# Kernel tuning notes

Measured on AMD Instinct MI355X. Metric: run time of the kernel, lower is better.

The kernel has to match this reference:

```python
import jax, jax.numpy as jnp
import numpy as np

N_NODES = 50000
N_EDGES = 800000
HID = 256
HEADS = 4
HEAD_C = HID // HEADS  # 64
IN_CH = 16
OUT_CH = 4
NEG_SLOPE = 0.2  # PyG GATConv default LeakyReLU slope
LN_EPS = 1e-5


def setup_inputs() -> dict:
    key = jax.random.key(0)
    ks = jax.random.split(key, 12)
    s = 0.05
    return {
        "x": jax.random.normal(ks[0], (N_NODES, IN_CH), dtype=jnp.float32),
        "edge_index": jax.random.randint(ks[1], (2, N_EDGES), 0, N_NODES, dtype=jnp.int64),
        "w_in": jax.random.normal(ks[2], (IN_CH, HID), dtype=jnp.float32) * s,
        "b_in": jnp.zeros((HID,), dtype=jnp.float32),
        "w_gat": jax.random.normal(ks[3], (4, HID, HID), dtype=jnp.float32) * s,
        "att_src": jax.random.normal(ks[4], (4, HEADS, HEAD_C), dtype=jnp.float32) * s,
        "att_dst": jax.random.normal(ks[5], (4, HEADS, HEAD_C), dtype=jnp.float32) * s,
        "b_gat": jnp.zeros((4, HID), dtype=jnp.float32),
        "ln_scale": jnp.ones((4, HID), dtype=jnp.float32),
        "ln_bias": jnp.zeros((4, HID), dtype=jnp.float32),
        "w_out": jax.random.normal(ks[6], (HID, OUT_CH), dtype=jnp.float32) * s,
        "b_out": jnp.zeros((OUT_CH,), dtype=jnp.float32),
    }


def _gat_layer(x, src, dst, W, a_src, a_dst, bias, g, beta):
    """One GATConv(concat, heads=4) + LayerNorm + ELU. x:[N,HID]."""
    n = x.shape[0]
    h = (x @ W).reshape(n, HEADS, HEAD_C)                 # [N,H,C]
    a_s = jnp.einsum("nhc,hc->nh", h, a_src)              # [N,H]
    a_d = jnp.einsum("nhc,hc->nh", h, a_dst)              # [N,H]
    logits = jax.nn.leaky_relu(a_s[src] + a_d[dst], NEG_SLOPE)  # [E,H]
    # segment softmax over destination neighborhoods (self-loops ensure non-empty)
    m = jax.ops.segment_max(logits, dst, num_segments=n)
    e = jnp.exp(logits - m[dst])
    denom = jax.ops.segment_sum(e, dst, num_segments=n)
    alpha = e / (denom[dst] + 1e-16)                      # [E,H]
    msg = alpha[:, :, None] * h[src]                      # [E,H,C]
    out = jax.ops.segment_sum(msg, dst, num_segments=n).reshape(n, HID) + bias
    mu = out.mean(-1, keepdims=True)
    var = out.var(-1, keepdims=True)
    out = (out - mu) * jax.lax.rsqrt(var + LN_EPS) * g + beta
    return jax.nn.elu(out)


def reference(x, edge_index, w_in, b_in, w_gat, att_src, att_dst, b_gat,
              ln_scale, ln_bias, w_out, b_out):
    n = x.shape[0]
    # PyG GATConv adds self-loops by default
    loops = jnp.arange(n, dtype=edge_index.dtype)
    ei = jnp.concatenate([edge_index, jnp.stack([loops, loops])], axis=1)
    src, dst = ei[0], ei[1]

    x = x @ w_in + b_in                                   # input_proj
    h = x
    for l in (0, 1):
        h = _gat_layer(h, src, dst, w_gat[l], att_src[l], att_dst[l],
                       b_gat[l], ln_scale[l], ln_bias[l])
    x = x + h
    h = x
    for l in (2, 3):
        h = _gat_layer(h, src, dst, w_gat[l], att_src[l], att_dst[l],
                       b_gat[l], ln_scale[l], ln_bias[l])
    x = x + h
    return x @ w_out + b_out
```

## Files before the change

kernel.cpp:

```cpp
#include <hip/hip_runtime.h>
#include <math.h>

#define NN 50000
#define E0 800000
#define ET 850000
#define HID 256
#define INCH 16
#define MAXDEG 64

#define NB_EDGE 3321
#define NB_WT   256
#define NB_IP   6250
#define NB_PREP (NB_EDGE + NB_WT + NB_IP)

typedef _Float16 h8 __attribute__((ext_vector_type(8)));
typedef float f32x4 __attribute__((ext_vector_type(4)));

__device__ __forceinline__ void load_lds16(const void* g, void* l) {
    __builtin_amdgcn_global_load_lds(
        (const __attribute__((address_space(1))) unsigned int*)g,
        (__attribute__((address_space(3))) unsigned int*)l, 16, 0, 0);
}

__global__ __launch_bounds__(256) void prep_kernel(
    const int* __restrict__ ei, int* __restrict__ cursor, int* __restrict__ csr_pad,
    const float* __restrict__ w_gat, _Float16* __restrict__ WT,
    const float* __restrict__ x, const float* __restrict__ w_in,
    const float* __restrict__ b_in, _Float16* __restrict__ Ph) {
    int b = blockIdx.x, t = threadIdx.x;
    if (b < NB_EDGE) {
        int e = b * 256 + t;
        if (e < ET) {
            int s, d;
            if (e < E0) { s = ei[e]; d = ei[E0 + e]; }
            else        { s = d = e - E0; }
            int pos = atomicAdd(&cursor[d], 1);
            if (pos < MAXDEG) csr_pad[(d << 6) + pos] = s;
        }
    } else if (b < NB_EDGE + NB_WT) {
        int k = b - NB_EDGE;
#pragma unroll
        for (int l = 0; l < 4; ++l) {
            float v = w_gat[((size_t)l * 256 + k) * 256 + t];
            WT[((size_t)l * 256 + t) * 256 + k] = (_Float16)v;
        }
    } else {
        int ipb = b - NB_EDGE - NB_WT;
        int sub = t >> 5, l32 = t & 31;
        int n = ipb * 8 + sub;
        int c0 = l32 * 8;
        const float* xr = x + n * INCH;
        float a[8];
#pragma unroll
        for (int k = 0; k < 8; k += 4) {
            float4 bb = *(const float4*)(b_in + c0 + k);
            a[k] = bb.x; a[k + 1] = bb.y; a[k + 2] = bb.z; a[k + 3] = bb.w;
        }
#pragma unroll
        for (int k = 0; k < INCH; ++k) {
            float xv = xr[k];
            const float4 w0 = *(const float4*)(w_in + k * 256 + c0);
            const float4 w1 = *(const float4*)(w_in + k * 256 + c0 + 4);
            a[0] += xv * w0.x; a[1] += xv * w0.y; a[2] += xv * w0.z; a[3] += xv * w0.w;
            a[4] += xv * w1.x; a[5] += xv * w1.y; a[6] += xv * w1.z; a[7] += xv * w1.w;
        }
        h8 o;
#pragma unroll
        for (int k = 0; k < 8; ++k) o[k] = (_Float16)a[k];
        *(h8*)(Ph + (size_t)n * 256 + c0) = o;
    }
}

__global__ __launch_bounds__(256) void gemm_fused_kernel(
    const _Float16* __restrict__ A, const _Float16* __restrict__ BT,
    _Float16* __restrict__ H, const float* __restrict__ att_s,
    const float* __restrict__ att_d, float* __restrict__ AS, float* __restrict__ AD,
    int N) {
    __shared__ _Float16 As[128 * 32];
    __shared__ _Float16 Bs[128 * 32];
    int t = threadIdx.x;
    int wv = t >> 6, lane = t & 63;
    int rb = blockIdx.x * 128, cb = blockIdx.y * 128;
    int wr = (wv >> 1) * 64, wc = (wv & 1) * 64;
    int lm = lane & 15, lq = lane >> 4;
    f32x4 acc[4][4] = {};

    int rch = lane >> 2;
    int q = lane & 3;

    for (int k0 = 0; k0 < 256; k0 += 32) {
#pragma unroll
        for (int c = 0; c < 2; ++c) {
            int r = wv * 32 + c * 16 + rch;
            int g = q ^ (r & 3);
            int ra = rb + r; if (ra >= N) ra = N - 1;
            load_lds16(A + (size_t)ra * 256 + k0 + g * 8,
                       (char*)As + wv * 2048 + c * 1024);
            load_lds16(BT + (size_t)(cb + r) * 256 + k0 + g * 8,
                       (char*)Bs + wv * 2048 + c * 1024);
        }
        __syncthreads();
        h8 af[4], bfr[4];
#pragma unroll
        for (int i = 0; i < 4; ++i) {
            int row = wr + i * 16 + lm;
            af[i] = *(const h8*)((const char*)As + row * 64 + ((lq ^ (row & 3)) * 16));
        }
#pragma unroll
        for (int j = 0; j < 4; ++j) {
            int row = wc + j * 16 + lm;
            bfr[j] = *(const h8*)((const char*)Bs + row * 64 + ((lq ^ (row & 3)) * 16));
        }
#pragma unroll
        for (int i = 0; i < 4; ++i)
#pragma unroll
            for (int j = 0; j < 4; ++j)
                acc[i][j] = __builtin_amdgcn_mfma_f32_16x16x32_f16(af[i], bfr[j], acc[i][j], 0, 0, 0);
        __syncthreads();
    }

    int head = (cb + wc) >> 6;
    float sa[4], sd[4];
#pragma unroll
    for (int j = 0; j < 4; ++j) {
        sa[j] = att_s[head * 64 + j * 16 + lm];
        sd[j] = att_d[head * 64 + j * 16 + lm];
    }
#pragma unroll
    for (int i = 0; i < 4; ++i)
#pragma unroll
        for (int rr = 0; rr < 4; ++rr) {
            float vs = acc[i][0][rr] * sa[0] + acc[i][1][rr] * sa[1]
                     + acc[i][2][rr] * sa[2] + acc[i][3][rr] * sa[3];
            float vd = acc[i][0][rr] * sd[0] + acc[i][1][rr] * sd[1]
                     + acc[i][2][rr] * sd[2] + acc[i][3][rr] * sd[3];
#pragma unroll
            for (int o = 1; o <= 8; o <<= 1) {
                vs += __shfl_xor(vs, o, 64);
                vd += __shfl_xor(vd, o, 64);
            }
            int row = rb + wr + i * 16 + lq * 4 + rr;
            if (lm == 0 && row < N) {
                AS[row * 4 + head] = vs;
                AD[row * 4 + head] = vd;
            }
        }

#pragma unroll
    for (int i = 0; i < 4; ++i)
#pragma unroll
        for (int j = 0; j < 4; ++j) {
            int col = cb + wc + j * 16 + lm;
#pragma unroll
            for (int rr = 0; rr < 4; ++rr) {
                int row = rb + wr + i * 16 + lq * 4 + rr;
                if (row < N) H[(size_t)row * 256 + col] = (_Float16)acc[i][j][rr];
            }
        }
}

__global__ __launch_bounds__(256) void agg_kernel(
    const _Float16* __restrict__ H, const float4* __restrict__ AS,
    const float4* __restrict__ AD,
    const int* __restrict__ cnt, const int* __restrict__ csr_pad,
    const float* __restrict__ bias, const float* __restrict__ g, const float* __restrict__ beta,
    const _Float16* __restrict__ res, _Float16* __restrict__ outh) {
    int t = threadIdx.x;
    int l32 = t & 31;
    int n = blockIdx.x * 8 + (t >> 5);
    int deg = cnt[n];
    if (deg > MAXDEG) deg = MAXDEG;
    int start = n << 6, end = start + deg;
    float4 adv = AD[n];
    int head = l32 >> 3;
    int c0 = l32 * 8;
    float advh = (head == 0) ? adv.x : (head == 1) ? adv.y : (head == 2) ? adv.z : adv.w;

    float acc[8] = {};
    float acc_e = 0.f;
#pragma unroll 4
    for (int i = start; i < end; ++i) {
        int s = csr_pad[i];
        const float* as = (const float*)&AS[s];
        float v = as[head] + advh;
        v = (v >= 0.f) ? v : 0.2f * v;
        float e = __expf(v);
        acc_e += e;
        h8 hv = *(const h8*)(H + (size_t)s * 256 + c0);
#pragma unroll
        for (int k = 0; k < 8; ++k) acc[k] += e * (float)hv[k];
    }
    float dinv = 1.f / (acc_e + 1e-16f);

    float val[8];
#pragma unroll
    for (int k = 0; k < 8; k += 4) {
        float4 bb = *(const float4*)(bias + c0 + k);
        val[k]     = acc[k]     * dinv + bb.x;
        val[k + 1] = acc[k + 1] * dinv + bb.y;
        val[k + 2] = acc[k + 2] * dinv + bb.z;
        val[k + 3] = acc[k + 3] * dinv + bb.w;
    }

    float s1 = 0.f, s2 = 0.f;
#pragma unroll
    for (int k = 0; k < 8; ++k) { s1 += val[k]; s2 += val[k] * val[k]; }
#pragma unroll
    for (int o = 16; o >= 1; o >>= 1) {
        s1 += __shfl_xor(s1, o, 64);
        s2 += __shfl_xor(s2, o, 64);
    }
    float mu = s1 * (1.f / 256.f);
    float var = s2 * (1.f / 256.f) - mu * mu;
    float rs = rsqrtf(var + 1e-5f);

    float y[8];
#pragma unroll
    for (int k = 0; k < 8; k += 4) {
        float4 g4 = *(const float4*)(g + c0 + k);
        float4 b4 = *(const float4*)(beta + c0 + k);
        y[k]     = (val[k]     - mu) * rs * g4.x + b4.x;
        y[k + 1] = (val[k + 1] - mu) * rs * g4.y + b4.y;
        y[k + 2] = (val[k + 2] - mu) * rs * g4.z + b4.z;
        y[k + 3] = (val[k + 3] - mu) * rs * g4.w + b4.w;
    }
#pragma unroll
    for (int k = 0; k < 8; ++k) y[k] = (y[k] > 0.f) ? y[k] : (__expf(y[k]) - 1.f);
    if (res) {
        h8 r0 = *(const h8*)(res + (size_t)n * 256 + c0);
#pragma unroll
        for (int k = 0; k < 8; ++k) y[k] += (float)r0[k];
    }
    h8 o0;
#pragma unroll
    for (int k = 0; k < 8; ++k) o0[k] = (_Float16)y[k];
    *(h8*)(outh + (size_t)n * 256 + c0) = o0;
}

__global__ __launch_bounds__(256) void out_proj_kernel(
    const _Float16* __restrict__ x, const float* __restrict__ w,
    const float* __restrict__ b, float* __restrict__ out, int n) {
    int tid = blockIdx.x * blockDim.x + threadIdx.x;
    int node = tid >> 6, lane = tid & 63;
    if (node >= n) return;
    const _Float16* xp = x + (size_t)node * HID + lane * 4;
    float x0 = (float)xp[0], x1 = (float)xp[1], x2 = (float)xp[2], x3 = (float)xp[3];
    const float4* wr = (const float4*)w;
    float4 w0 = wr[lane * 4 + 0];
    float4 w1 = wr[lane * 4 + 1];
    float4 w2 = wr[lane * 4 + 2];
    float4 w3 = wr[lane * 4 + 3];
    float o0 = x0 * w0.x + x1 * w1.x + x2 * w2.x + x3 * w3.x;
    float o1 = x0 * w0.y + x1 * w1.y + x2 * w2.y + x3 * w3.y;
    float o2 = x0 * w0.z + x1 * w1.z + x2 * w2.z + x3 * w3.z;
    float o3 = x0 * w0.w + x1 * w1.w + x2 * w2.w + x3 * w3.w;
#pragma unroll
    for (int o = 32; o >= 1; o >>= 1) {
        o0 += __shfl_down(o0, o, 64);
        o1 += __shfl_down(o1, o, 64);
        o2 += __shfl_down(o2, o, 64);
        o3 += __shfl_down(o3, o, 64);
    }
    if (lane == 0) {
        out[node * 4 + 0] = o0 + b[0];
        out[node * 4 + 1] = o1 + b[1];
        out[node * 4 + 2] = o2 + b[2];
        out[node * 4 + 3] = o3 + b[3];
    }
}

extern "C" void kernel_launch(void* const* d_in, const int* in_sizes, int n_in,
                              void* d_out, int out_size, void* d_ws, size_t ws_size,
                              hipStream_t stream) {
    const float* x       = (const float*)d_in[0];
    const int*   ei      = (const int*)  d_in[1];
    const float* w_in    = (const float*)d_in[2];
    const float* b_in    = (const float*)d_in[3];
    const float* w_gat   = (const float*)d_in[4];
    const float* att_src = (const float*)d_in[5];
    const float* att_dst = (const float*)d_in[6];
    const float* b_gat   = (const float*)d_in[7];
    const float* ln_g    = (const float*)d_in[8];
    const float* ln_b    = (const float*)d_in[9];
    const float* w_out   = (const float*)d_in[10];
    const float* b_out   = (const float*)d_in[11];
    float* out = (float*)d_out;

    char* ws = (char*)d_ws;
    size_t off = 0;
    auto alloc = [&](size_t bytes) {
        void* p = ws + off;
        off += (bytes + 255) & ~(size_t)255;
        return p;
    };
    _Float16*  Ph      = (_Float16*)alloc((size_t)NN * HID * 2);
    _Float16*  Ch      = (_Float16*)alloc((size_t)NN * HID * 2);
    _Float16*  Gh      = (_Float16*)alloc((size_t)NN * HID * 2);
    _Float16*  H       = (_Float16*)alloc((size_t)NN * HID * 2);
    _Float16*  WT      = (_Float16*)alloc((size_t)4 * HID * HID * 2);
    float*     ASAD    = (float*)alloc((size_t)NN * 8 * 4);
    int*       cursor  = (int*)alloc((size_t)NN * 4);
    int*       csr_pad = (int*)alloc((size_t)NN * MAXDEG * 4);

    float* AS = ASAD;
    float* AD = ASAD + (size_t)NN * 4;

    const dim3 GEMM_GRID((NN + 127) / 128, 2);
    const int NB_AGG = NN / 8;

    hipMemsetAsync(cursor, 0, (size_t)NN * 4, stream);
    prep_kernel<<<NB_PREP, 256, 0, stream>>>(ei, cursor, csr_pad, w_gat, WT,
                                             x, w_in, b_in, Ph);

    auto run_layer = [&](const _Float16* inh, int l, const _Float16* res, _Float16* outh) {
        gemm_fused_kernel<<<GEMM_GRID, 256, 0, stream>>>(
            inh, WT + (size_t)l * HID * HID, H,
            att_src + l * 256, att_dst + l * 256, AS, AD, NN);
        agg_kernel<<<NB_AGG, 256, 0, stream>>>(
            H, (const float4*)AS, (const float4*)AD, cursor, csr_pad,
            b_gat + l * 256, ln_g + l * 256, ln_b + l * 256, res, outh);
    };

    run_layer(Ph, 0, nullptr, Gh);
    run_layer(Gh, 1, Ph,      Ch);
    run_layer(Ch, 2, nullptr, Gh);
    run_layer(Gh, 3, Ch,      Ph);

    out_proj_kernel<<<(NN * 64 + 255) / 256, 256, 0, stream>>>(Ph, w_out, b_out, out, NN);
}
```

Before: 547.1 us.

## Fuse edge scatter into first GEMM, fuse output projection into last aggregation

Zeroing of the degree cursor moves from a memset into the prep kernel. The edge-scatter CSR build is moved out of prep into the layer-0 GEMM launch as extra blocks, so the scatter atomics overlap with the GEMM tiles. The output projection is folded into the final aggregation kernel, which no longer writes the fp16 hidden state. Together these remove a memset, one kernel launch and a full read/write of the 50000x256 activations, but the combined kernels now hold mixed workloads.

```diff
diff --git a/kernel.cpp b/kernel.cpp
--- a/kernel.cpp
+++ b/kernel.cpp
@@ -8,10 +8,14 @@
 #define INCH 16
 #define MAXDEG 64
 
-#define NB_EDGE 3321
+#define NB_Z    49
 #define NB_WT   256
 #define NB_IP   6250
-#define NB_PREP (NB_EDGE + NB_WT + NB_IP)
+#define NB_PREP (NB_Z + NB_WT + NB_IP)
+
+#define NB_G    782
+#define NB_EDGE 3321
+#define NB_G0   (NB_G + NB_EDGE)
 
 typedef _Float16 h8 __attribute__((ext_vector_type(8)));
 typedef float f32x4 __attribute__((ext_vector_type(4)));
@@ -23,13 +27,155 @@
 }
 
 __global__ __launch_bounds__(256) void prep_kernel(
-    const int* __restrict__ ei, int* __restrict__ cursor, int* __restrict__ csr_pad,
+    int* __restrict__ cursor,
     const float* __restrict__ w_gat, _Float16* __restrict__ WT,
     const float* __restrict__ x, const float* __restrict__ w_in,
     const float* __restrict__ b_in, _Float16* __restrict__ Ph) {
     int b = blockIdx.x, t = threadIdx.x;
-    if (b < NB_EDGE) {
-        int e = b * 256 + t;
+    if (b < NB_Z) {
+        int i = (b * 256 + t) * 4;
+#pragma unroll
+        for (int k = 0; k < 4; ++k)
+            if (i + k < NN) cursor[i + k] = 0;
+    } else if (b < NB_Z + NB_WT) {
+        int k = b - NB_Z;
+#pragma unroll
+        for (int l = 0; l < 4; ++l) {
+            float v = w_gat[((size_t)l * 256 + k) * 256 + t];
+            WT[((size_t)l * 256 + t) * 256 + k] = (_Float16)v;
+        }
+    } else {
+        int ipb = b - NB_Z - NB_WT;
+        int sub = t >> 5, l32 = t & 31;
+        int n = ipb * 8 + sub;
+        int c0 = l32 * 8;
+        const float* xr = x + n * INCH;
+        float a[8];
+#pragma unroll
+        for (int k = 0; k < 8; k += 4) {
+            float4 bb = *(const float4*)(b_in + c0 + k);
+            a[k] = bb.x; a[k + 1] = bb.y; a[k + 2] = bb.z; a[k + 3] = bb.w;
+        }
+#pragma unroll
+        for (int k = 0; k < INCH; ++k) {
+            float xv = xr[k];
+            const float4 w0 = *(const float4*)(w_in + k * 256 + c0);
+            const float4 w1 = *(const float4*)(w_in + k * 256 + c0 + 4);
+            a[0] += xv * w0.x; a[1] += xv * w0.y; a[2] += xv * w0.z; a[3] += xv * w0.w;
+            a[4] += xv * w1.x; a[5] += xv * w1.y; a[6] += xv * w1.z; a[7] += xv * w1.w;
+        }
+        h8 o;
+#pragma unroll
+        for (int k = 0; k < 8; ++k) o[k] = (_Float16)a[k];
+        *(h8*)(Ph + (size_t)n * 256 + c0) = o;
+    }
+}
+
+__device__ __forceinline__ void gemm_tile(
+    int rb, int cb,
+    const _Float16* __restrict__ A, const _Float16* __restrict__ BT,
+    _Float16* __restrict__ H, const float* __restrict__ att_s,
+    const float* __restrict__ att_d, float* __restrict__ AS, float* __restrict__ AD,
+    _Float16* As, _Float16* Bs) {
+    int t = threadIdx.x;
+    int wv = t >> 6, lane = t & 63;
+    int wr = (wv >> 1) * 64, wc = (wv & 1) * 64;
+    int lm = lane & 15, lq = lane >> 4;
+    f32x4 acc[4][4] = {};
+
+    int rch = lane >> 2;
+    int q = lane & 3;
+
+    for (int k0 = 0; k0 < 256; k0 += 32) {
+#pragma unroll
+        for (int c = 0; c < 2; ++c) {
+            int r = wv * 32 + c * 16 + rch;
+            int g = q ^ (r & 3);
+            int ra = rb + r; if (ra >= NN) ra = NN - 1;
+            load_lds16(A + (size_t)ra * 256 + k0 + g * 8,
+                       (char*)As + wv * 2048 + c * 1024);
+            load_lds16(BT + (size_t)(cb + r) * 256 + k0 + g * 8,
+                       (char*)Bs + wv * 2048 + c * 1024);
+        }
+        __syncthreads();
+        h8 af[4], bfr[4];
+#pragma unroll
+        for (int i = 0; i < 4; ++i) {
+            int row = wr + i * 16 + lm;
+            af[i] = *(const h8*)((const char*)As + row * 64 + ((lq ^ (row & 3)) * 16));
+        }
+#pragma unroll
+        for (int j = 0; j < 4; ++j) {
+            int row = wc + j * 16 + lm;
+            bfr[j] = *(const h8*)((const char*)Bs + row * 64 + ((lq ^ (row & 3)) * 16));
+        }
+#pragma unroll
+        for (int i = 0; i < 4; ++i)
+#pragma unroll
+            for (int j = 0; j < 4; ++j)
+                acc[i][j] = __builtin_amdgcn_mfma_f32_16x16x32_f16(af[i], bfr[j], acc[i][j], 0, 0, 0);
+        __syncthreads();
+    }
+
+    int head = (cb + wc) >> 6;
+    float sa[4], sd[4];
+#pragma unroll
+    for (int j = 0; j < 4; ++j) {
+        sa[j] = att_s[head * 64 + j * 16 + lm];
+        sd[j] = att_d[head * 64 + j * 16 + lm];
+    }
+#pragma unroll
+    for (int i = 0; i < 4; ++i)
+#pragma unroll
+        for (int rr = 0; rr < 4; ++rr) {
+            float vs = acc[i][0][rr] * sa[0] + acc[i][1][rr] * sa[1]
+                     + acc[i][2][rr] * sa[2] + acc[i][3][rr] * sa[3];
+            float vd = acc[i][0][rr] * sd[0] + acc[i][1][rr] * sd[1]
+                     + acc[i][2][rr] * sd[2] + acc[i][3][rr] * sd[3];
+#pragma unroll
+            for (int o = 1; o <= 8; o <<= 1) {
+                vs += __shfl_xor(vs, o, 64);
+                vd += __shfl_xor(vd, o, 64);
+            }
+            int row = rb + wr + i * 16 + lq * 4 + rr;
+            if (lm == 0 && row < NN) {
+                AS[row * 4 + head] = vs;
+                AD[row * 4 + head] = vd;
+            }
+        }
+
+#pragma unroll
+    for (int i = 0; i < 4; ++i)
+#pragma unroll
+        for (int j = 0; j < 4; ++j) {
+            int col = cb + wc + j * 16 + lm;
+#pragma unroll
+            for (int rr = 0; rr < 4; ++rr) {
+                int row = rb + wr + i * 16 + lq * 4 + rr;
+                if (row < NN) H[(size_t)row * 256 + col] = (_Float16)acc[i][j][rr];
+            }
+        }
+}
+
+__global__ __launch_bounds__(256) void gemm_fused_kernel(
+    const _Float16* __restrict__ A, const _Float16* __restrict__ BT,
+    _Float16* __restrict__ H, const float* __restrict__ att_s,
+    const float* __restrict__ att_d, float* __restrict__ AS, float* __restrict__ AD) {
+    __shared__ _Float16 As[128 * 32];
+    __shared__ _Float16 Bs[128 * 32];
+    gemm_tile(blockIdx.x * 128, blockIdx.y * 128, A, BT, H, att_s, att_d, AS, AD, As, Bs);
+}
+
+__global__ __launch_bounds__(256) void gemm0_scatter_kernel(
+    const _Float16* __restrict__ A, const _Float16* __restrict__ BT,
+    _Float16* __restrict__ H, const float* __restrict__ att_s,
+    const float* __restrict__ att_d, float* __restrict__ AS, float* __restrict__ AD,
+    const int* __restrict__ ei, int* __restrict__ cursor, int* __restrict__ csr_pad) {
+    __shared__ _Float16 As[128 * 32];
+    __shared__ _Float16 Bs[128 * 32];
+    int b = blockIdx.x;
+    if (b >= NB_G) {
+        int e = (b - NB_G) * 256 + threadIdx.x;
         if (e < ET) {
             int s, d;
             if (e < E0) { s = ei[e]; d = ei[E0 + e]; }
@@ -37,126 +183,9 @@
             int pos = atomicAdd(&cursor[d], 1);
             if (pos < MAXDEG) csr_pad[(d << 6) + pos] = s;
         }
-    } else if (b < NB_EDGE + NB_WT) {
-        int k = b - NB_EDGE;
-#pragma unroll
-        for (int l = 0; l < 4; ++l) {
-            float v = w_gat[((size_t)l * 256 + k) * 256 + t];
-            WT[((size_t)l * 256 + t) * 256 + k] = (_Float16)v;
-        }
-    } else {
-        int ipb = b - NB_EDGE - NB_WT;
-        int sub = t >> 5, l32 = t & 31;
-        int n = ipb * 8 + sub;
-        int c0 = l32 * 8;
-        const float* xr = x + n * INCH;
-        float a[8];
-#pragma unroll
-        for (int k = 0; k < 8; k += 4) {
-            float4 bb = *(const float4*)(b_in + c0 + k);
-            a[k] = bb.x; a[k + 1] = bb.y; a[k + 2] = bb.z; a[k + 3] = bb.w;
-        }
-#pragma unroll
-        for (int k = 0; k < INCH; ++k) {
-            float xv = xr[k];
-            const float4 w0 = *(const float4*)(w_in + k * 256 + c0);
-            const float4 w1 = *(const float4*)(w_in + k * 256 + c0 + 4);
-            a[0] += xv * w0.x; a[1] += xv * w0.y; a[2] += xv * w0.z; a[3] += xv * w0.w;
-            a[4] += xv * w1.x; a[5] += xv * w1.y; a[6] += xv * w1.z; a[7] += xv * w1.w;
-        }
-        h8 o;
-#pragma unroll
-        for (int k = 0; k < 8; ++k) o[k] = (_Float16)a[k];
-        *(h8*)(Ph + (size_t)n * 256 + c0) = o;
-    }
-}
-
-__global__ __launch_bounds__(256) void gemm_fused_kernel(
-    const _Float16* __restrict__ A, const _Float16* __restrict__ BT,
-    _Float16* __restrict__ H, const float* __restrict__ att_s,
-    const float* __restrict__ att_d, float* __restrict__ AS, float* __restrict__ AD,
-    int N) {
-    __shared__ _Float16 As[128 * 32];
-    __shared__ _Float16 Bs[128 * 32];
-    int t = threadIdx.x;
-    int wv = t >> 6, lane = t & 63;
-    int rb = blockIdx.x * 128, cb = blockIdx.y * 128;
-    int wr = (wv >> 1) * 64, wc = (wv & 1) * 64;
-    int lm = lane & 15, lq = lane >> 4;
-    f32x4 acc[4][4] = {};
-
-    int rch = lane >> 2;
-    int q = lane & 3;
-
-    for (int k0 = 0; k0 < 256; k0 += 32) {
-#pragma unroll
-        for (int c = 0; c < 2; ++c) {
-            int r = wv * 32 + c * 16 + rch;
-            int g = q ^ (r & 3);
-            int ra = rb + r; if (ra >= N) ra = N - 1;
-            load_lds16(A + (size_t)ra * 256 + k0 + g * 8,
-                       (char*)As + wv * 2048 + c * 1024);
-            load_lds16(BT + (size_t)(cb + r) * 256 + k0 + g * 8,
-                       (char*)Bs + wv * 2048 + c * 1024);
-        }
-        __syncthreads();
-        h8 af[4], bfr[4];
-#pragma unroll
-        for (int i = 0; i < 4; ++i) {
-            int row = wr + i * 16 + lm;
-            af[i] = *(const h8*)((const char*)As + row * 64 + ((lq ^ (row & 3)) * 16));
-        }
-#pragma unroll
-        for (int j = 0; j < 4; ++j) {
-            int row = wc + j * 16 + lm;
-            bfr[j] = *(const h8*)((const char*)Bs + row * 64 + ((lq ^ (row & 3)) * 16));
-        }
-#pragma unroll
-        for (int i = 0; i < 4; ++i)
-#pragma unroll
-            for (int j = 0; j < 4; ++j)
-                acc[i][j] = __builtin_amdgcn_mfma_f32_16x16x32_f16(af[i], bfr[j], acc[i][j], 0, 0, 0);
-        __syncthreads();
-    }
-
-    int head = (cb + wc) >> 6;
-    float sa[4], sd[4];
-#pragma unroll
-    for (int j = 0; j < 4; ++j) {
-        sa[j] = att_s[head * 64 + j * 16 + lm];
-        sd[j] = att_d[head * 64 + j * 16 + lm];
-    }
-#pragma unroll
-    for (int i = 0; i < 4; ++i)
-#pragma unroll
-        for (int rr = 0; rr < 4; ++rr) {
-            float vs = acc[i][0][rr] * sa[0] + acc[i][1][rr] * sa[1]
-                     + acc[i][2][rr] * sa[2] + acc[i][3][rr] * sa[3];
-            float vd = acc[i][0][rr] * sd[0] + acc[i][1][rr] * sd[1]
-                     + acc[i][2][rr] * sd[2] + acc[i][3][rr] * sd[3];
-#pragma unroll
-            for (int o = 1; o <= 8; o <<= 1) {
-                vs += __shfl_xor(vs, o, 64);
-                vd += __shfl_xor(vd, o, 64);
-            }
-            int row = rb + wr + i * 16 + lq * 4 + rr;
-            if (lm == 0 && row < N) {
-                AS[row * 4 + head] = vs;
-                AD[row * 4 + head] = vd;
-            }
-        }
-
-#pragma unroll
-    for (int i = 0; i < 4; ++i)
-#pragma unroll
-        for (int j = 0; j < 4; ++j) {
-            int col = cb + wc + j * 16 + lm;
-#pragma unroll
-            for (int rr = 0; rr < 4; ++rr) {
-                int row = rb + wr + i * 16 + lq * 4 + rr;
-                if (row < N) H[(size_t)row * 256 + col] = (_Float16)acc[i][j][rr];
-            }
-        }
+        return;
+    }
+    gemm_tile((b >> 1) * 128, (b & 1) * 128, A, BT, H, att_s, att_d, AS, AD, As, Bs);
 }
 
 __global__ __launch_bounds__(256) void agg_kernel(
@@ -164,7 +193,9 @@
     const float4* __restrict__ AD,
     const int* __restrict__ cnt, const int* __restrict__ csr_pad,
     const float* __restrict__ bias, const float* __restrict__ g, const float* __restrict__ beta,
-    const _Float16* __restrict__ res, _Float16* __restrict__ outh) {
+    const _Float16* __restrict__ res, _Float16* __restrict__ outh,
+    const float* __restrict__ wout, const float* __restrict__ bout,
+    float* __restrict__ out) {
     int t = threadIdx.x;
     int l32 = t & 31;
     int n = blockIdx.x * 8 + (t >> 5);
@@ -231,41 +262,29 @@
 #pragma unroll
         for (int k = 0; k < 8; ++k) y[k] += (float)r0[k];
     }
-    h8 o0;
-#pragma unroll
-    for (int k = 0; k < 8; ++k) o0[k] = (_Float16)y[k];
-    *(h8*)(outh + (size_t)n * 256 + c0) = o0;
-}
-
-__global__ __launch_bounds__(256) void out_proj_kernel(
-    const _Float16* __restrict__ x, const float* __restrict__ w,
-    const float* __restrict__ b, float* __restrict__ out, int n) {
-    int tid = blockIdx.x * blockDim.x + threadIdx.x;
-    int node = tid >> 6, lane = tid & 63;
-    if (node >= n) return;
-    const _Float16* xp = x + (size_t)node * HID + lane * 4;
-    float x0 = (float)xp[0], x1 = (float)xp[1], x2 = (float)xp[2], x3 = (float)xp[3];
-    const float4* wr = (const float4*)w;
-    float4 w0 = wr[lane * 4 + 0];
-    float4 w1 = wr[lane * 4 + 1];
-    float4 w2 = wr[lane * 4 + 2];
-    float4 w3 = wr[lane * 4 + 3];
-    float o0 = x0 * w0.x + x1 * w1.x + x2 * w2.x + x3 * w3.x;
-    float o1 = x0 * w0.y + x1 * w1.y + x2 * w2.y + x3 * w3.y;
-    float o2 = x0 * w0.z + x1 * w1.z + x2 * w2.z + x3 * w3.z;
-    float o3 = x0 * w0.w + x1 * w1.w + x2 * w2.w + x3 * w3.w;
-#pragma unroll
-    for (int o = 32; o >= 1; o >>= 1) {
-        o0 += __shfl_down(o0, o, 64);
-        o1 += __shfl_down(o1, o, 64);
-        o2 += __shfl_down(o2, o, 64);
-        o3 += __shfl_down(o3, o, 64);
-    }
-    if (lane == 0) {
-        out[node * 4 + 0] = o0 + b[0];
-        out[node * 4 + 1] = o1 + b[1];
-        out[node * 4 + 2] = o2 + b[2];
-        out[node * 4 + 3] = o3 + b[3];
+    if (wout) {
+        float o0 = 0.f, o1 = 0.f, o2 = 0.f, o3 = 0.f;
+#pragma unroll
+        for (int k = 0; k < 8; ++k) {
+            float4 wv = *(const float4*)(wout + (size_t)(c0 + k) * 4);
+            o0 += y[k] * wv.x; o1 += y[k] * wv.y; o2 += y[k] * wv.z; o3 += y[k] * wv.w;
+        }
+#pragma unroll
+        for (int o = 16; o >= 1; o >>= 1) {
+            o0 += __shfl_xor(o0, o, 64);
+            o1 += __shfl_xor(o1, o, 64);
+            o2 += __shfl_xor(o2, o, 64);
+            o3 += __shfl_xor(o3, o, 64);
+        }
+        if (l32 == 0) {
+            float4 ov = make_float4(o0 + bout[0], o1 + bout[1], o2 + bout[2], o3 + bout[3]);
+            *(float4*)(out + (size_t)n * 4) = ov;
+        }
+    } else {
+        h8 o0;
+#pragma unroll
+        for (int k = 0; k < 8; ++k) o0[k] = (_Float16)y[k];
+        *(h8*)(outh + (size_t)n * 256 + c0) = o0;
     }
 }
 
@@ -305,26 +324,29 @@
     float* AS = ASAD;
     float* AD = ASAD + (size_t)NN * 4;
 
-    const dim3 GEMM_GRID((NN + 127) / 128, 2);
+    const dim3 GEMM_GRID(391, 2);
     const int NB_AGG = NN / 8;
 
-    hipMemsetAsync(cursor, 0, (size_t)NN * 4, stream);
-    prep_kernel<<<NB_PREP, 256, 0, stream>>>(ei, cursor, csr_pad, w_gat, WT,
-                                             x, w_in, b_in, Ph);
-
-    auto run_layer = [&](const _Float16* inh, int l, const _Float16* res, _Float16* outh) {
+    prep_kernel<<<NB_PREP, 256, 0, stream>>>(cursor, w_gat, WT, x, w_in, b_in, Ph);
+
+    gemm0_scatter_kernel<<<NB_G0, 256, 0, stream>>>(
+        Ph, WT, H, att_src, att_dst, AS, AD, ei, cursor, csr_pad);
+    agg_kernel<<<NB_AGG, 256, 0, stream>>>(
+        H, (const float4*)AS, (const float4*)AD, cursor, csr_pad,
+        b_gat, ln_g, ln_b, nullptr, Gh, nullptr, nullptr, nullptr);
+
+    auto run_layer = [&](const _Float16* inh, int l, const _Float16* res, _Float16* outh,
+                         const float* wo, const float* bo) {
         gemm_fused_kernel<<<GEMM_GRID, 256, 0, stream>>>(
             inh, WT + (size_t)l * HID * HID, H,
-            att_src + l * 256, att_dst + l * 256, AS, AD, NN);
+            att_src + l * 256, att_dst + l * 256, AS, AD);
         agg_kernel<<<NB_AGG, 256, 0, stream>>>(
             H, (const float4*)AS, (const float4*)AD, cursor, csr_pad,
-            b_gat + l * 256, ln_g + l * 256, ln_b + l * 256, res, outh);
+            b_gat + l * 256, ln_g + l * 256, ln_b + l * 256, res, outh, wo, bo,
+            wo ? out : nullptr);
     };
 
-    run_layer(Ph, 0, nullptr, Gh);
-    run_layer(Gh, 1, Ph,      Ch);
-    run_layer(Ch, 2, nullptr, Gh);
-    run_layer(Gh, 3, Ch,      Ph);
-
-    out_proj_kernel<<<(NN * 64 + 255) / 256, 256, 0, stream>>>(Ph, w_out, b_out, out, NN);
-}
+    run_layer(Gh, 1, Ph,      Ch, nullptr, nullptr);
+    run_layer(Ch, 2, nullptr, Gh, nullptr, nullptr);
+    run_layer(Gh, 3, Ch,      Ph, w_out,   b_out);
+}
```

Result: faster. 522.5 us (-4.5%).
